# Optimization experiments

Hardware: AMD Instinct MI355X
Metric: run time of the kernel (lower is better)

Reference implementation:

```python
import jax, jax.numpy as jnp
import numpy as np

N_ATOMS = 131072
N_MOLS = 4096
D = 128
N_DEPTH = 128
EPS = 1e-07
MEMBERSHIPS = np.array([(-1.645, 0.283), (-1.08, 0.17), (-0.739, 0.134), (-0.468, 0.118),
                        (-0.228, 0.114), (0.0, 0.114), (0.228, 0.114), (0.468, 0.118),
                        (0.739, 0.134), (1.08, 0.17), (1.645, 0.283)], dtype=np.float32)


def setup_inputs() -> dict:
    key = jax.random.key(0)
    k1, k2, k3, k4 = jax.random.split(key, 4)
    x = jax.random.normal(k1, (N_ATOMS, D), dtype=jnp.float32)
    atom_split = jnp.sort(jax.random.randint(k2, (N_ATOMS,), 0, N_MOLS)).astype(jnp.int64)
    W = jax.random.normal(k3, (D * 11, N_DEPTH), dtype=jnp.float32) * 0.02
    b = jax.random.normal(k4, (N_DEPTH,), dtype=jnp.float32) * 0.02
    return {"x": x, "atom_split": atom_split, "W": W, "b": b}


def reference(x, atom_split, W, b):
    means = jnp.asarray(MEMBERSHIPS[:, 0])          # [11]
    stds = jnp.asarray(MEMBERSHIPS[:, 1])           # [11]
    log_norm = jnp.log(stds * np.sqrt(2.0 * np.pi)) # [11]
    # Normal log_prob: -0.5*((x-m)/s)^2 - log(s*sqrt(2pi)); dist_max = log_prob(m) = -log_norm
    z = (x[:, :, None] - means) / stds              # [N, D, 11]
    logp = -0.5 * z * z - log_norm
    out = logp / (-log_norm)                        # divide by log_prob at mean
    out = (out + EPS) / (jnp.sum(out, axis=2, keepdims=True) + EPS)
    out = out.reshape(-1, D * 11)                   # [N, D*11]
    mols = jax.ops.segment_sum(out, atom_split, num_segments=N_MOLS)  # [M, D*11]
    return jnp.tanh(mols @ W + b)                   # [M, n_depth]
```

## Files before the change

kernel.cpp:

```cpp
#include <hip/hip_runtime.h>
#include <math.h>

#define N_ATOMS 131072
#define N_MOLS  4096
#define DFEAT   128
#define NK      11
#define KDIM3   384
#define N_DEPTH 128
#define EPS_F   1e-7f
#define MPB     8
#define TPB     512
#define SCAN_BLOCKS (N_ATOMS / 256)

__constant__ float c_means[NK] = {-1.645f, -1.08f, -0.739f, -0.468f, -0.228f,
                                  0.0f, 0.228f, 0.468f, 0.739f, 1.08f, 1.645f};
__constant__ float c_stds[NK]  = {0.283f, 0.17f, 0.134f, 0.118f, 0.114f,
                                  0.114f, 0.114f, 0.118f, 0.134f, 0.17f, 0.283f};


__global__ __launch_bounds__(256) void wxform_offsets_kernel(
    const float* __restrict__ W,
    const int*   __restrict__ split,
    float*       __restrict__ Bt,
    int*         __restrict__ offsets) {
  const int bid = blockIdx.x;
  const int tid = threadIdx.x;
  if (bid < 192) {
    int t = bid * 256 + tid;
    int n = t & 127;
    int row = t >> 7;
    int j = row >> 7;
    int d = row & 127;
    float acc = 0.0f;
#pragma unroll
    for (int k = 0; k < NK; ++k) {
      float m = c_means[k], s = c_stds[k];
      float a = 0.5f / (s * s * logf(s * 2.5066282746310002f));
      float coef = (j == 2) ? a
                 : (j == 1) ? (-2.0f * a * m)
                            : fmaf(a, m * m, 1.0f + EPS_F);
      acc = fmaf(coef, W[(size_t)(d * NK + k) * N_DEPTH + n], acc);
    }
    Bt[(size_t)row * N_DEPTH + n] = acc;
  } else {
    int a = (bid - 192) * 256 + tid;
    int cur  = split[a];
    int prev = (a == 0) ? -1 : split[a - 1];
    for (int j = prev + 1; j <= cur; ++j) offsets[j] = a;
    if (a == N_ATOMS - 1)
      for (int j = cur + 1; j <= N_MOLS; ++j) offsets[j] = N_ATOMS;
  }
}

__global__ __launch_bounds__(TPB, 8) void fused_sums_gemm_kernel(
    const float* __restrict__ x,
    const int*   __restrict__ offsets,
    const float* __restrict__ Bt,
    const float* __restrict__ bias,
    float*       __restrict__ out) {
  const int tid = threadIdx.x;
  const int m0  = blockIdx.x * MPB;

  __shared__ float As[MPB][KDIM3];
  __shared__ float comb[4][MPB][DFEAT];

  float C2 = 0.0f, C1 = 0.0f, C0 = 11.0f + EPS_F;
#pragma unroll
  for (int k = 0; k < NK; ++k) {
    float m_ = c_means[k], s_ = c_stds[k];
    float a = 0.5f / (s_ * s_ * logf(s_ * 2.5066282746310002f));
    C2 += a;
    C1 = fmaf(-2.0f * a, m_, C1);
    C0 = fmaf(a, m_ * m_, C0);
  }

  const int w    = tid >> 6;
  const int lane = tid & 63;
  const int fq   = lane & 31;
  const int h    = lane >> 5;

  const int start = offsets[m0 + w];
  const int end   = offsets[m0 + w + 1];

  float Sr[4]   = {0.f, 0.f, 0.f, 0.f};
  float Sxr[4]  = {0.f, 0.f, 0.f, 0.f};
  float Sxxr[4] = {0.f, 0.f, 0.f, 0.f};

  const float* xp = x + fq * 4;

  auto proc = [&](float4 v) {
    float xv[4] = {v.x, v.y, v.z, v.w};
#pragma unroll
    for (int q = 0; q < 4; ++q) {
      float den = fmaf(fmaf(C2, xv[q], C1), xv[q], C0);
      float r   = __builtin_amdgcn_rcpf(den);
      float u   = xv[q] * r;
      Sr[q]  += r;
      Sxr[q] += u;
      Sxxr[q] = fmaf(xv[q], u, Sxxr[q]);
    }
  };

  int a = start + h;
  for (; a + 6 < end; a += 8) {
    float4 v0 = *(const float4*)&xp[(size_t)(a + 0) * DFEAT];
    float4 v1 = *(const float4*)&xp[(size_t)(a + 2) * DFEAT];
    float4 v2 = *(const float4*)&xp[(size_t)(a + 4) * DFEAT];
    float4 v3 = *(const float4*)&xp[(size_t)(a + 6) * DFEAT];
    proc(v0); proc(v1); proc(v2); proc(v3);
  }
  for (; a < end; a += 2) {
    float4 v = *(const float4*)&xp[(size_t)a * DFEAT];
    proc(v);
  }

#pragma unroll
  for (int q = 0; q < 4; ++q) {
    Sr[q]   += __shfl_xor(Sr[q],   32, 64);
    Sxr[q]  += __shfl_xor(Sxr[q],  32, 64);
    Sxxr[q] += __shfl_xor(Sxxr[q], 32, 64);
  }

  if (h == 0) {
    *(float4*)&As[w][fq * 4]             = make_float4(Sr[0],  Sr[1],  Sr[2],  Sr[3]);
    *(float4*)&As[w][DFEAT + fq * 4]     = make_float4(Sxr[0], Sxr[1], Sxr[2], Sxr[3]);
    *(float4*)&As[w][2 * DFEAT + fq * 4] = make_float4(Sxxr[0],Sxxr[1],Sxxr[2],Sxxr[3]);
  }
  __syncthreads();

  const int n  = tid & 127;
  const int hh = tid >> 7;
  const int kbase = hh * (KDIM3 / 4);

  float pacc[MPB];
#pragma unroll
  for (int i = 0; i < MPB; ++i) pacc[i] = 0.0f;

#pragma unroll 2
  for (int kk = 0; kk < KDIM3 / 4; kk += 4) {
    int k = kbase + kk;
    float b0 = Bt[(size_t)(k + 0) * N_DEPTH + n];
    float b1 = Bt[(size_t)(k + 1) * N_DEPTH + n];
    float b2 = Bt[(size_t)(k + 2) * N_DEPTH + n];
    float b3 = Bt[(size_t)(k + 3) * N_DEPTH + n];
#pragma unroll
    for (int i = 0; i < MPB; ++i) {
      float4 av = *(const float4*)&As[i][k];
      pacc[i] = fmaf(av.x, b0, pacc[i]);
      pacc[i] = fmaf(av.y, b1, pacc[i]);
      pacc[i] = fmaf(av.z, b2, pacc[i]);
      pacc[i] = fmaf(av.w, b3, pacc[i]);
    }
  }

#pragma unroll
  for (int i = 0; i < MPB; ++i) comb[hh][i][n] = pacc[i];
  __syncthreads();

#pragma unroll
  for (int off = 0; off < (MPB * DFEAT) / TPB; ++off) {
    int idx = off * TPB + tid;
    int i  = idx >> 7;
    int nn = idx & 127;
    float v = comb[0][i][nn] + comb[1][i][nn] + comb[2][i][nn] + comb[3][i][nn]
            + bias[nn];
    out[(size_t)(m0 + i) * N_DEPTH + nn] = tanhf(v);
  }
}

extern "C" void kernel_launch(void* const* d_in, const int* in_sizes, int n_in,
                              void* d_out, int out_size, void* d_ws, size_t ws_size,
                              hipStream_t stream) {
  const float* x     = (const float*)d_in[0];
  const int*   split = (const int*)d_in[1];
  const float* W     = (const float*)d_in[2];
  const float* bias  = (const float*)d_in[3];
  float* out = (float*)d_out;

  float* Bt      = (float*)d_ws;
  int*   offsets = (int*)((char*)d_ws + (size_t)KDIM3 * N_DEPTH * 4);

  wxform_offsets_kernel<<<dim3(192 + SCAN_BLOCKS), dim3(256), 0, stream>>>(W, split, Bt, offsets);
  fused_sums_gemm_kernel<<<dim3(N_MOLS / MPB), dim3(TPB), 0, stream>>>(x, offsets, Bt, bias, out);
}
```

Measured before the change: 112.7 us.

## Split fused segment-sum and GEMM into separate kernels via workspace

The fused sums+GEMM kernel becomes two kernels. The first computes per-molecule moment sums into a global workspace, using 256-thread blocks of 4 molecules. The second does the GEMM with bias and tanh, reading those sums through wave-uniform scalar pointers. This drops the shared-memory staging, the syncthreads barriers and the cross-wave reduction, and allows smaller blocks for the streaming pass. The cost is an extra launch plus a global write and read of the 4096x384 sums array.

```diff
diff --git a/kernel.cpp b/kernel.cpp
--- a/kernel.cpp
+++ b/kernel.cpp
@@ -8,8 +8,6 @@
 #define KDIM3   384
 #define N_DEPTH 128
 #define EPS_F   1e-7f
-#define MPB     8
-#define TPB     512
 #define SCAN_BLOCKS (N_ATOMS / 256)
 
 __constant__ float c_means[NK] = {-1.645f, -1.08f, -0.739f, -0.468f, -0.228f,
@@ -52,17 +50,16 @@
   }
 }
 
-__global__ __launch_bounds__(TPB, 8) void fused_sums_gemm_kernel(
+__global__ __launch_bounds__(256, 8) void sums_kernel(
     const float* __restrict__ x,
     const int*   __restrict__ offsets,
-    const float* __restrict__ Bt,
-    const float* __restrict__ bias,
-    float*       __restrict__ out) {
-  const int tid = threadIdx.x;
-  const int m0  = blockIdx.x * MPB;
-
-  __shared__ float As[MPB][KDIM3];
-  __shared__ float comb[4][MPB][DFEAT];
+    float*       __restrict__ S) {
+  const int tid  = threadIdx.x;
+  const int w    = tid >> 6;
+  const int lane = tid & 63;
+  const int fq   = lane & 31;
+  const int h    = lane >> 5;
+  const int mol  = blockIdx.x * 4 + w;
 
   float C2 = 0.0f, C1 = 0.0f, C0 = 11.0f + EPS_F;
 #pragma unroll
@@ -74,13 +71,8 @@
     C0 = fmaf(a, m_ * m_, C0);
   }
 
-  const int w    = tid >> 6;
-  const int lane = tid & 63;
-  const int fq   = lane & 31;
-  const int h    = lane >> 5;
-
-  const int start = offsets[m0 + w];
-  const int end   = offsets[m0 + w + 1];
+  const int start = offsets[mol];
+  const int end   = offsets[mol + 1];
 
   float Sr[4]   = {0.f, 0.f, 0.f, 0.f};
   float Sxr[4]  = {0.f, 0.f, 0.f, 0.f};
@@ -122,49 +114,51 @@
   }
 
   if (h == 0) {
-    *(float4*)&As[w][fq * 4]             = make_float4(Sr[0],  Sr[1],  Sr[2],  Sr[3]);
-    *(float4*)&As[w][DFEAT + fq * 4]     = make_float4(Sxr[0], Sxr[1], Sxr[2], Sxr[3]);
-    *(float4*)&As[w][2 * DFEAT + fq * 4] = make_float4(Sxxr[0],Sxxr[1],Sxxr[2],Sxxr[3]);
+    float* Sp = S + (size_t)mol * KDIM3;
+    *(float4*)&Sp[fq * 4]             = make_float4(Sr[0],  Sr[1],  Sr[2],  Sr[3]);
+    *(float4*)&Sp[DFEAT + fq * 4]     = make_float4(Sxr[0], Sxr[1], Sxr[2], Sxr[3]);
+    *(float4*)&Sp[2 * DFEAT + fq * 4] = make_float4(Sxxr[0],Sxxr[1],Sxxr[2],Sxxr[3]);
   }
-  __syncthreads();
+}
 
-  const int n  = tid & 127;
-  const int hh = tid >> 7;
-  const int kbase = hh * (KDIM3 / 4);
+__global__ __launch_bounds__(256) void gemm_bias_tanh_kernel(
+    const float* __restrict__ S,
+    const float* __restrict__ Bt,
+    const float* __restrict__ bias,
+    float*       __restrict__ out) {
+  const int tid  = threadIdx.x;
+  const int n    = tid & 127;
+  const int isub = tid >> 7;
+  const int m0   = blockIdx.x * 8;
 
-  float pacc[MPB];
+  const float* Sp[4];
 #pragma unroll
-  for (int i = 0; i < MPB; ++i) pacc[i] = 0.0f;
+  for (int j = 0; j < 4; ++j) {
+    int molu = __builtin_amdgcn_readfirstlane(m0 + isub * 4 + j);
+    Sp[j] = S + (size_t)molu * KDIM3;
+  }
 
-#pragma unroll 2
-  for (int kk = 0; kk < KDIM3 / 4; kk += 4) {
-    int k = kbase + kk;
-    float b0 = Bt[(size_t)(k + 0) * N_DEPTH + n];
-    float b1 = Bt[(size_t)(k + 1) * N_DEPTH + n];
-    float b2 = Bt[(size_t)(k + 2) * N_DEPTH + n];
-    float b3 = Bt[(size_t)(k + 3) * N_DEPTH + n];
+  float acc[4] = {0.f, 0.f, 0.f, 0.f};
+
+#pragma unroll 1
+  for (int kt = 0; kt < KDIM3; kt += 8) {
+    float b[8];
 #pragma unroll
-    for (int i = 0; i < MPB; ++i) {
-      float4 av = *(const float4*)&As[i][k];
-      pacc[i] = fmaf(av.x, b0, pacc[i]);
-      pacc[i] = fmaf(av.y, b1, pacc[i]);
-      pacc[i] = fmaf(av.z, b2, pacc[i]);
-      pacc[i] = fmaf(av.w, b3, pacc[i]);
+    for (int t = 0; t < 8; ++t)
+      b[t] = Bt[(size_t)(kt + t) * N_DEPTH + n];
+#pragma unroll
+    for (int j = 0; j < 4; ++j) {
+#pragma unroll
+      for (int t = 0; t < 8; ++t)
+        acc[j] = fmaf(Sp[j][kt + t], b[t], acc[j]);
     }
   }
 
+  float bv = bias[n];
 #pragma unroll
-  for (int i = 0; i < MPB; ++i) comb[hh][i][n] = pacc[i];
-  __syncthreads();
-
-#pragma unroll
-  for (int off = 0; off < (MPB * DFEAT) / TPB; ++off) {
-    int idx = off * TPB + tid;
-    int i  = idx >> 7;
-    int nn = idx & 127;
-    float v = comb[0][i][nn] + comb[1][i][nn] + comb[2][i][nn] + comb[3][i][nn]
-            + bias[nn];
-    out[(size_t)(m0 + i) * N_DEPTH + nn] = tanhf(v);
+  for (int j = 0; j < 4; ++j) {
+    int row = m0 + isub * 4 + j;
+    out[(size_t)row * N_DEPTH + n] = tanhf(acc[j] + bv);
   }
 }
 
@@ -177,9 +171,11 @@
   const float* bias  = (const float*)d_in[3];
   float* out = (float*)d_out;
 
-  float* Bt      = (float*)d_ws;
-  int*   offsets = (int*)((char*)d_ws + (size_t)KDIM3 * N_DEPTH * 4);
+  float* S       = (float*)d_ws;
+  float* Bt      = (float*)((char*)d_ws + (size_t)N_MOLS * KDIM3 * 4);
+  int*   offsets = (int*)((char*)Bt + (size_t)KDIM3 * N_DEPTH * 4);
 
   wxform_offsets_kernel<<<dim3(192 + SCAN_BLOCKS), dim3(256), 0, stream>>>(W, split, Bt, offsets);
-  fused_sums_gemm_kernel<<<dim3(N_MOLS / MPB), dim3(TPB), 0, stream>>>(x, offsets, Bt, bias, out);
+  sums_kernel<<<dim3(N_MOLS / 4), dim3(256), 0, stream>>>(x, offsets, S);
+  gemm_bias_tanh_kernel<<<dim3(N_MOLS / 8), dim3(256), 0, stream>>>(S, Bt, bias, out);
 }
```

Measured after the change: 121.1 us. 7.5% more time.
